# Performance work log

Hardware: AMD Instinct MI355X
Metric: run time of the kernel (lower is better)

Reference implementation:

```python
import jax, jax.numpy as jnp
import numpy as np

N = 32              # num_nodes
E = N * (N - 1)     # 992 directed edges
K = 2               # edge_types
D = 4               # n_in_node
H = 64              # msg_hid
M = 64              # msg_out
NH = 128            # n_hid
B, T = 8, 256


def setup_inputs() -> dict:
    key = jax.random.key(0)
    ks = jax.random.split(key, 14)
    # one-hot gather/scatter matrices over all ordered node pairs (i != j)
    pairs = np.array([(i, j) for i in range(N) for j in range(N) if i != j])
    eye = np.eye(N, dtype=np.float32)
    rel_rec = jnp.asarray(eye[pairs[:, 0]])   # [E, N] receiver one-hot
    rel_send = jnp.asarray(eye[pairs[:, 1]])  # [E, N] sender one-hot
    inputs = jax.random.normal(ks[0], (B, N, T, D), dtype=jnp.float32)
    s = 0.1
    return {
        "inputs": inputs,
        "rel_rec": rel_rec,
        "rel_send": rel_send,
        "rel_graph": jax.random.normal(ks[1], (1, 1, E, K), jnp.float32) * s,
        "W1": jax.random.normal(ks[2], (K, 2 * D, H), jnp.float32) * s,
        "b1": jnp.zeros((K, H), jnp.float32),
        "W2": jax.random.normal(ks[3], (K, H, M), jnp.float32) * s,
        "b2": jnp.zeros((K, M), jnp.float32),
        "Wo1": jax.random.normal(ks[4], (D + M, NH), jnp.float32) * s,
        "bo1": jnp.zeros((NH,), jnp.float32),
        "Wo2": jax.random.normal(ks[5], (NH, NH), jnp.float32) * s,
        "bo2": jnp.zeros((NH,), jnp.float32),
        "Wo3": jax.random.normal(ks[6], (NH, D), jnp.float32) * s,
        "bo3": jnp.zeros((D,), jnp.float32),
        "tau": 1,
        "hard": 1,
        "pred_steps": 1,
    }


def _single_step(x, rel_rec, rel_send, rel_graph, W1, b1, W2, b2,
                 Wo1, bo1, Wo2, bo2, Wo3, bo3):
    # x: [B, Tsub, N, D]
    receivers = jnp.einsum("en,btnd->bted", rel_rec, x)
    senders = jnp.einsum("en,btnd->bted", rel_send, x)
    pre_msg = jnp.concatenate([senders, receivers], axis=-1)  # [B,Tsub,E,2D]
    all_msgs = jnp.zeros(pre_msg.shape[:3] + (M,), pre_msg.dtype)
    for k in range(K):  # small fixed edge-type loop (dropout is identity, p=0)
        msg = jax.nn.relu(pre_msg @ W1[k] + b1[k])
        msg = jax.nn.relu(msg @ W2[k] + b2[k])          # [B,Tsub,E,M]
        all_msgs = all_msgs + msg * rel_graph[:, :, :, k:k + 1]
    # scatter back to receiver nodes: [B,Tsub,N,M]
    agg_msgs = jnp.einsum("btem,en->btnm", all_msgs, rel_rec)
    aug = jnp.concatenate([x, agg_msgs], axis=-1)
    pred = jax.nn.relu(aug @ Wo1 + bo1)
    pred = jax.nn.relu(pred @ Wo2 + bo2)
    pred = pred @ Wo3 + bo3
    return x + pred


def reference(inputs, rel_rec, rel_send, rel_graph, W1, b1, W2, b2,
              Wo1, bo1, Wo2, bo2, Wo3, bo3, tau, hard, pred_steps):
    # NOTE: original computes gumbel_softmax(rel_graph, tau, hard) but never
    # uses the result in the math, so tau/hard are inert here.
    x = jnp.transpose(inputs, (0, 2, 1, 3))  # [B, T, N, D]
    time_steps = x.shape[1]
    last_pred = x[:, ::pred_steps]           # [B, L, N, D]
    preds = []
    for _ in range(pred_steps):
        last_pred = _single_step(last_pred, rel_rec, rel_send, rel_graph,
                                 W1, b1, W2, b2, Wo1, bo1, Wo2, bo2, Wo3, bo3)
        preds.append(last_pred)
    Bx, L, Nn, Dd = preds[0].shape
    # interleave: output[:, i::pred_steps] = preds[i]
    output = jnp.stack(preds, axis=2).reshape(Bx, L * pred_steps, Nn, Dd)
    pred_all = output[:, : time_steps - 1]
    pred_all = jnp.transpose(pred_all, (0, 2, 1, 3))  # [B, N, T-1, D]
    rel_graph_out = jnp.broadcast_to(rel_graph[:, 0], (inputs.shape[0], E, K))
    return (pred_all, rel_graph_out)
```

## Files before the change

### kernel.cpp

```cpp
#include <hip/hip_runtime.h>


typedef _Float16     f16x8 __attribute__((ext_vector_type(8)));
typedef float        f32x4 __attribute__((ext_vector_type(4)));
typedef unsigned int u32x4 __attribute__((ext_vector_type(4)));

static __device__ __forceinline__ f16x8 pack8(float a0, float b0, float a1, float b1,
                                              float a2, float b2, float a3, float b3)
{
    u32x4 u;
    u.x = __builtin_bit_cast(unsigned int, __builtin_amdgcn_cvt_pkrtz(a0, b0));
    u.y = __builtin_bit_cast(unsigned int, __builtin_amdgcn_cvt_pkrtz(a1, b1));
    u.z = __builtin_bit_cast(unsigned int, __builtin_amdgcn_cvt_pkrtz(a2, b2));
    u.w = __builtin_bit_cast(unsigned int, __builtin_amdgcn_cvt_pkrtz(a3, b3));
    return __builtin_bit_cast(f16x8, u);
}

__global__ __launch_bounds__(256, 3)
void nri_fused(const float* __restrict__ inputs,
               const float* __restrict__ rgraph,
               const float* __restrict__ W1,  const float* __restrict__ b1,
               const float* __restrict__ W2,  const float* __restrict__ b2,
               const float* __restrict__ Wo1, const float* __restrict__ bo1,
               const float* __restrict__ Wo2, const float* __restrict__ bo2,
               const float* __restrict__ Wo3, const float* __restrict__ bo3,
               float* __restrict__ out)
{
    __shared__ float smem[11968];
    float* x_l = smem;
    float* g_l = smem + 128;
    float* S   = smem + 2112;
    float* R   = smem + 4288;
    float* aug = smem + 6464;
    _Float16* w2t = reinterpret_cast<_Float16*>(smem + 9664);
    _Float16* h_l = reinterpret_cast<_Float16*>(smem + 9664);
    float* p2  = smem + 2112;

    const int tid  = threadIdx.x;
    const int b    = blockIdx.x >> 8;
    const int t    = blockIdx.x & 255;
    const int w    = tid >> 6;
    const int lane = tid & 63;
    const int q    = lane & 15;
    const int g4   = lane >> 4;

    if (tid < 32)
        reinterpret_cast<float4*>(x_l)[tid] =
            *reinterpret_cast<const float4*>(inputs + ((size_t)(b * 32 + tid) * 256 + t) * 4);
    for (int idx = tid; idx < 1984; idx += 256) g_l[idx] = rgraph[idx];
    for (int idx = tid; idx < 1024; idx += 256) {
        const int n = idx >> 5, c = idx & 31;
        aug[n * 100 + 64 + c] =
            (c < 4) ? inputs[((size_t)(b * 32 + n) * 256 + t) * 4 + c] : 0.f;
    }

    float agg_acc[8];
    #pragma unroll
    for (int rr = 0; rr < 8; ++rr) agg_acc[rr] = 0.f;

    for (int k = 0; k < 2; ++k) {
        __syncthreads();
        for (int idx = tid; idx < 2048; idx += 256) {
            const int j = idx >> 6, kk = idx & 63;
            const float4 xj = reinterpret_cast<const float4*>(x_l)[j];
            const float* wp = W1 + k * 512 + kk;
            float s = b1[k * 64 + kk], r = 0.f;
            s = fmaf(xj.x, wp[0],   s);  r = fmaf(xj.x, wp[256], r);
            s = fmaf(xj.y, wp[64],  s);  r = fmaf(xj.y, wp[320], r);
            s = fmaf(xj.z, wp[128], s);  r = fmaf(xj.z, wp[384], r);
            s = fmaf(xj.w, wp[192], s);  r = fmaf(xj.w, wp[448], r);
            S[j * 68 + kk] = s;
            R[j * 68 + kk] = r;
        }
        for (int idx = tid; idx < 4096; idx += 256) {
            const int kk = idx >> 6, m = idx & 63;
            w2t[m * 72 + kk] = (_Float16)W2[k * 4096 + idx];
        }
        float bb[4];
        #pragma unroll
        for (int n = 0; n < 4; ++n) bb[n] = b2[k * 64 + 16 * n + q];
        __syncthreads();

        #pragma unroll
        for (int rr = 0; rr < 8; ++rr) {
            const int i = w * 8 + rr;
            f32x4 acc[2][4];
            #pragma unroll
            for (int m = 0; m < 2; ++m)
                #pragma unroll
                for (int n = 0; n < 4; ++n) {
                    acc[m][n][0] = bb[n]; acc[m][n][1] = bb[n];
                    acc[m][n][2] = bb[n]; acc[m][n][3] = bb[n];
                }
            #pragma unroll
            for (int s = 0; s < 2; ++s) {
                const float* rp = R + i * 68 + 32 * s + 8 * g4;
                const float4 Rv0 = *reinterpret_cast<const float4*>(rp);
                const float4 Rv1 = *reinterpret_cast<const float4*>(rp + 4);
                f16x8 af[2];
                #pragma unroll
                for (int m = 0; m < 2; ++m) {
                    const int r = 16 * m + q;
                    const int j = (r == 31) ? 0 : ((r < i) ? r : r + 1);
                    const float* sp = S + j * 68 + 32 * s + 8 * g4;
                    const float4 s0 = *reinterpret_cast<const float4*>(sp);
                    const float4 s1 = *reinterpret_cast<const float4*>(sp + 4);
                    af[m] = pack8(
                        fmaxf(s0.x + Rv0.x, 0.f), fmaxf(s0.y + Rv0.y, 0.f),
                        fmaxf(s0.z + Rv0.z, 0.f), fmaxf(s0.w + Rv0.w, 0.f),
                        fmaxf(s1.x + Rv1.x, 0.f), fmaxf(s1.y + Rv1.y, 0.f),
                        fmaxf(s1.z + Rv1.z, 0.f), fmaxf(s1.w + Rv1.w, 0.f));
                }
                #pragma unroll
                for (int n = 0; n < 4; ++n) {
                    const f16x8 wb = *reinterpret_cast<const f16x8*>(
                        w2t + (16 * n + q) * 72 + 32 * s + 8 * g4);
                    acc[0][n] = __builtin_amdgcn_mfma_f32_16x16x32_f16(
                        af[0], wb, acc[0][n], 0, 0, 0);
                    acc[1][n] = __builtin_amdgcn_mfma_f32_16x16x32_f16(
                        af[1], wb, acc[1][n], 0, 0, 0);
                }
            }
            float part[4] = {0.f, 0.f, 0.f, 0.f};
            #pragma unroll
            for (int m = 0; m < 2; ++m)
                #pragma unroll
                for (int reg = 0; reg < 4; ++reg) {
                    const int row = 16 * m + 4 * g4 + reg;
                    const float gv = (row < 31) ? g_l[(31 * i + row) * 2 + k] : 0.f;
                    #pragma unroll
                    for (int n = 0; n < 4; ++n)
                        part[n] = fmaf(fmaxf(acc[m][n][reg], 0.f), gv, part[n]);
                }
            #pragma unroll
            for (int n = 0; n < 4; ++n) {
                part[n] += __shfl_xor(part[n], 16);
                part[n] += __shfl_xor(part[n], 32);
            }
            const float v = (g4 == 0) ? part[0] : (g4 == 1) ? part[1]
                          : (g4 == 2) ? part[2] : part[3];
            agg_acc[rr] += v;
        }
    }

    #pragma unroll
    for (int rr = 0; rr < 8; ++rr)
        aug[(w * 8 + rr) * 100 + 16 * g4 + q] = agg_acc[rr];
    __syncthreads();

    const int c0 = 32 * w;

    {
        f16x8 bf[2][3];
        #pragma unroll
        for (int n = 0; n < 2; ++n)
            #pragma unroll
            for (int s = 0; s < 3; ++s) {
                const int col = c0 + 16 * n + q;
                const int ka = 32 * s + 8 * g4;
                float vv[8];
                #pragma unroll
                for (int e2 = 0; e2 < 8; ++e2) {
                    const int kx = ka + e2;
                    vv[e2] = (kx < 64) ? Wo1[(4 + kx) * 128 + col]
                           : ((kx < 68) ? Wo1[(kx - 64) * 128 + col] : 0.f);
                }
                bf[n][s] = pack8(vv[0], vv[1], vv[2], vv[3], vv[4], vv[5], vv[6], vv[7]);
            }
        f32x4 acc[2][2];
        #pragma unroll
        for (int m = 0; m < 2; ++m)
            #pragma unroll
            for (int n = 0; n < 2; ++n) {
                const float bv = bo1[c0 + 16 * n + q];
                acc[m][n][0] = bv; acc[m][n][1] = bv; acc[m][n][2] = bv; acc[m][n][3] = bv;
            }
        #pragma unroll
        for (int s = 0; s < 3; ++s) {
            f16x8 afr[2];
            #pragma unroll
            for (int m = 0; m < 2; ++m) {
                const float* ap = aug + (16 * m + q) * 100 + 32 * s + 8 * g4;
                const float4 a0 = *reinterpret_cast<const float4*>(ap);
                const float4 a1 = *reinterpret_cast<const float4*>(ap + 4);
                afr[m] = pack8(a0.x, a0.y, a0.z, a0.w, a1.x, a1.y, a1.z, a1.w);
            }
            #pragma unroll
            for (int m = 0; m < 2; ++m)
                #pragma unroll
                for (int n = 0; n < 2; ++n)
                    acc[m][n] = __builtin_amdgcn_mfma_f32_16x16x32_f16(
                        afr[m], bf[n][s], acc[m][n], 0, 0, 0);
        }
        __syncthreads();
        #pragma unroll
        for (int m = 0; m < 2; ++m)
            #pragma unroll
            for (int n = 0; n < 2; ++n)
                #pragma unroll
                for (int reg = 0; reg < 4; ++reg) {
                    const int row = 16 * m + 4 * g4 + reg;
                    h_l[row * 136 + c0 + 16 * n + q] = (_Float16)fmaxf(acc[m][n][reg], 0.f);
                }
    }
    __syncthreads();

    {
        f16x8 bf[2][4];
        #pragma unroll
        for (int n = 0; n < 2; ++n)
            #pragma unroll
            for (int s = 0; s < 4; ++s) {
                const int col = c0 + 16 * n + q;
                const int ka = 32 * s + 8 * g4;
                bf[n][s] = pack8(Wo2[(ka + 0) * 128 + col], Wo2[(ka + 1) * 128 + col],
                                 Wo2[(ka + 2) * 128 + col], Wo2[(ka + 3) * 128 + col],
                                 Wo2[(ka + 4) * 128 + col], Wo2[(ka + 5) * 128 + col],
                                 Wo2[(ka + 6) * 128 + col], Wo2[(ka + 7) * 128 + col]);
            }
        f32x4 acc[2][2];
        #pragma unroll
        for (int m = 0; m < 2; ++m)
            #pragma unroll
            for (int n = 0; n < 2; ++n) {
                const float bv = bo2[c0 + 16 * n + q];
                acc[m][n][0] = bv; acc[m][n][1] = bv; acc[m][n][2] = bv; acc[m][n][3] = bv;
            }
        #pragma unroll
        for (int s = 0; s < 4; ++s) {
            f16x8 afr[2];
            #pragma unroll
            for (int m = 0; m < 2; ++m)
                afr[m] = *reinterpret_cast<const f16x8*>(
                    h_l + (16 * m + q) * 136 + 32 * s + 8 * g4);
            #pragma unroll
            for (int m = 0; m < 2; ++m)
                #pragma unroll
                for (int n = 0; n < 2; ++n)
                    acc[m][n] = __builtin_amdgcn_mfma_f32_16x16x32_f16(
                        afr[m], bf[n][s], acc[m][n], 0, 0, 0);
        }
        #pragma unroll
        for (int m = 0; m < 2; ++m)
            #pragma unroll
            for (int n = 0; n < 2; ++n)
                #pragma unroll
                for (int reg = 0; reg < 4; ++reg) {
                    const int row = 16 * m + 4 * g4 + reg;
                    p2[row * 132 + c0 + 16 * n + q] = fmaxf(acc[m][n][reg], 0.f);
                }
    }
    __syncthreads();

    if (tid < 128 && t < 255) {
        const int rr3 = tid >> 2;
        const int dd  = tid & 3;
        float a0 = 0.f, a1 = 0.f, a2 = 0.f, a3 = 0.f;
        const float* pr = p2 + rr3 * 132;
        for (int d = 0; d < 128; d += 4) {
            a0 = fmaf(pr[d + 0], Wo3[(d + 0) * 4 + dd], a0);
            a1 = fmaf(pr[d + 1], Wo3[(d + 1) * 4 + dd], a1);
            a2 = fmaf(pr[d + 2], Wo3[(d + 2) * 4 + dd], a2);
            a3 = fmaf(pr[d + 3], Wo3[(d + 3) * 4 + dd], a3);
        }
        const float pred = ((a0 + a1) + (a2 + a3)) + bo3[dd];
        out[((size_t)(b * 32 + rr3) * 255 + t) * 4 + dd] = x_l[rr3 * 4 + dd] + pred;
    }
}

__global__ void copy_relgraph(const float* __restrict__ g, float* __restrict__ out2)
{
    const int idx = blockIdx.x * 256 + threadIdx.x;
    if (idx < 15872) out2[idx] = g[idx % 1984];
}

extern "C" void kernel_launch(void* const* d_in, const int* in_sizes, int n_in,
                              void* d_out, int out_size, void* d_ws, size_t ws_size,
                              hipStream_t stream)
{
    (void)in_sizes; (void)n_in; (void)d_ws; (void)ws_size; (void)out_size;
    const float* inputs    = (const float*)d_in[0];
    const float* rel_graph = (const float*)d_in[3];
    const float* W1  = (const float*)d_in[4];
    const float* b1  = (const float*)d_in[5];
    const float* W2  = (const float*)d_in[6];
    const float* b2  = (const float*)d_in[7];
    const float* Wo1 = (const float*)d_in[8];
    const float* bo1 = (const float*)d_in[9];
    const float* Wo2 = (const float*)d_in[10];
    const float* bo2 = (const float*)d_in[11];
    const float* Wo3 = (const float*)d_in[12];
    const float* bo3 = (const float*)d_in[13];
    float* out = (float*)d_out;

    nri_fused<<<2048, 256, 0, stream>>>(inputs, rel_graph, W1, b1, W2, b2,
                                        Wo1, bo1, Wo2, bo2, Wo3, bo3, out);
    copy_relgraph<<<62, 256, 0, stream>>>(rel_graph, out + 261120);
}
```

Measured before the change: 183.6 us.

## Shrink LDS and split MFMA accumulators to raise occupancy to four blocks

Raises launch bounds from 3 to 4 blocks per CU and shrinks shared memory. The rel_graph weights are now stored as fp16, and the aug buffer no longer holds the raw input columns; the last K-slice of the first output MLP instead reads x directly from x_l. The message MLP's second layer is split into two halves of output columns, so only 4 accumulators are live at once instead of 8, which cuts register pressure. A __syncthreads is removed. Risks include fp16 rounding of the graph weights and possible spills or a race from the removed barrier, since h_l aliases w2t.

Result: slower. 223.4 us (+21.7%).

```diff
diff --git a/kernel.cpp b/kernel.cpp
--- a/kernel.cpp
+++ b/kernel.cpp
@@ -16,7 +16,7 @@
     return __builtin_bit_cast(f16x8, u);
 }
 
-__global__ __launch_bounds__(256, 3)
+__global__ __launch_bounds__(256, 4)
 void nri_fused(const float* __restrict__ inputs,
                const float* __restrict__ rgraph,
                const float* __restrict__ W1,  const float* __restrict__ b1,
@@ -26,15 +26,15 @@
                const float* __restrict__ Wo3, const float* __restrict__ bo3,
                float* __restrict__ out)
 {
-    __shared__ float smem[11968];
+    __shared__ float smem[9952];
     float* x_l = smem;
-    float* g_l = smem + 128;
-    float* S   = smem + 2112;
-    float* R   = smem + 4288;
-    float* aug = smem + 6464;
-    _Float16* w2t = reinterpret_cast<_Float16*>(smem + 9664);
-    _Float16* h_l = reinterpret_cast<_Float16*>(smem + 9664);
-    float* p2  = smem + 2112;
+    _Float16* g16 = reinterpret_cast<_Float16*>(smem + 128);
+    float* S   = smem + 1120;
+    float* R   = smem + 3296;
+    float* aug = smem + 5472;
+    _Float16* w2t = reinterpret_cast<_Float16*>(smem + 7648);
+    _Float16* h_l = reinterpret_cast<_Float16*>(smem + 7648);
+    float* p2  = smem + 1120;
 
     const int tid  = threadIdx.x;
     const int b    = blockIdx.x >> 8;
@@ -47,12 +47,7 @@
     if (tid < 32)
         reinterpret_cast<float4*>(x_l)[tid] =
             *reinterpret_cast<const float4*>(inputs + ((size_t)(b * 32 + tid) * 256 + t) * 4);
-    for (int idx = tid; idx < 1984; idx += 256) g_l[idx] = rgraph[idx];
-    for (int idx = tid; idx < 1024; idx += 256) {
-        const int n = idx >> 5, c = idx & 31;
-        aug[n * 100 + 64 + c] =
-            (c < 4) ? inputs[((size_t)(b * 32 + n) * 256 + t) * 4 + c] : 0.f;
-    }
+    for (int idx = tid; idx < 1984; idx += 256) g16[idx] = (_Float16)rgraph[idx];
 
     float agg_acc[8];
     #pragma unroll
@@ -84,20 +79,12 @@
         #pragma unroll
         for (int rr = 0; rr < 8; ++rr) {
             const int i = w * 8 + rr;
-            f32x4 acc[2][4];
-            #pragma unroll
-            for (int m = 0; m < 2; ++m)
-                #pragma unroll
-                for (int n = 0; n < 4; ++n) {
-                    acc[m][n][0] = bb[n]; acc[m][n][1] = bb[n];
-                    acc[m][n][2] = bb[n]; acc[m][n][3] = bb[n];
-                }
+            f16x8 af[2][2];
             #pragma unroll
             for (int s = 0; s < 2; ++s) {
                 const float* rp = R + i * 68 + 32 * s + 8 * g4;
                 const float4 Rv0 = *reinterpret_cast<const float4*>(rp);
                 const float4 Rv1 = *reinterpret_cast<const float4*>(rp + 4);
-                f16x8 af[2];
                 #pragma unroll
                 for (int m = 0; m < 2; ++m) {
                     const int r = 16 * m + q;
@@ -105,33 +92,57 @@
                     const float* sp = S + j * 68 + 32 * s + 8 * g4;
                     const float4 s0 = *reinterpret_cast<const float4*>(sp);
                     const float4 s1 = *reinterpret_cast<const float4*>(sp + 4);
-                    af[m] = pack8(
+                    af[m][s] = pack8(
                         fmaxf(s0.x + Rv0.x, 0.f), fmaxf(s0.y + Rv0.y, 0.f),
                         fmaxf(s0.z + Rv0.z, 0.f), fmaxf(s0.w + Rv0.w, 0.f),
                         fmaxf(s1.x + Rv1.x, 0.f), fmaxf(s1.y + Rv1.y, 0.f),
                         fmaxf(s1.z + Rv1.z, 0.f), fmaxf(s1.w + Rv1.w, 0.f));
                 }
-                #pragma unroll
-                for (int n = 0; n < 4; ++n) {
-                    const f16x8 wb = *reinterpret_cast<const f16x8*>(
-                        w2t + (16 * n + q) * 72 + 32 * s + 8 * g4);
-                    acc[0][n] = __builtin_amdgcn_mfma_f32_16x16x32_f16(
-                        af[0], wb, acc[0][n], 0, 0, 0);
-                    acc[1][n] = __builtin_amdgcn_mfma_f32_16x16x32_f16(
-                        af[1], wb, acc[1][n], 0, 0, 0);
-                }
-            }
-            float part[4] = {0.f, 0.f, 0.f, 0.f};
+            }
+            float gvr[8];
             #pragma unroll
             for (int m = 0; m < 2; ++m)
                 #pragma unroll
                 for (int reg = 0; reg < 4; ++reg) {
                     const int row = 16 * m + 4 * g4 + reg;
-                    const float gv = (row < 31) ? g_l[(31 * i + row) * 2 + k] : 0.f;
+                    gvr[m * 4 + reg] =
+                        (row < 31) ? (float)g16[(31 * i + row) * 2 + k] : 0.f;
+                }
+            float part[4];
+            #pragma unroll
+            for (int nh = 0; nh < 2; ++nh) {
+                f32x4 acc[2][2];
+                #pragma unroll
+                for (int m = 0; m < 2; ++m)
                     #pragma unroll
-                    for (int n = 0; n < 4; ++n)
-                        part[n] = fmaf(fmaxf(acc[m][n][reg], 0.f), gv, part[n]);
-                }
+                    for (int n2 = 0; n2 < 2; ++n2) {
+                        const float bv = bb[2 * nh + n2];
+                        acc[m][n2][0] = bv; acc[m][n2][1] = bv;
+                        acc[m][n2][2] = bv; acc[m][n2][3] = bv;
+                    }
+                #pragma unroll
+                for (int s = 0; s < 2; ++s)
+                    #pragma unroll
+                    for (int n2 = 0; n2 < 2; ++n2) {
+                        const f16x8 wb = *reinterpret_cast<const f16x8*>(
+                            w2t + (16 * (2 * nh + n2) + q) * 72 + 32 * s + 8 * g4);
+                        acc[0][n2] = __builtin_amdgcn_mfma_f32_16x16x32_f16(
+                            af[0][s], wb, acc[0][n2], 0, 0, 0);
+                        acc[1][n2] = __builtin_amdgcn_mfma_f32_16x16x32_f16(
+                            af[1][s], wb, acc[1][n2], 0, 0, 0);
+                    }
+                float p0 = 0.f, p1 = 0.f;
+                #pragma unroll
+                for (int m = 0; m < 2; ++m)
+                    #pragma unroll
+                    for (int reg = 0; reg < 4; ++reg) {
+                        const float gv = gvr[m * 4 + reg];
+                        p0 = fmaf(fmaxf(acc[m][0][reg], 0.f), gv, p0);
+                        p1 = fmaf(fmaxf(acc[m][1][reg], 0.f), gv, p1);
+                    }
+                part[2 * nh + 0] = p0;
+                part[2 * nh + 1] = p1;
+            }
             #pragma unroll
             for (int n = 0; n < 4; ++n) {
                 part[n] += __shfl_xor(part[n], 16);
@@ -145,7 +156,7 @@
 
     #pragma unroll
     for (int rr = 0; rr < 8; ++rr)
-        aug[(w * 8 + rr) * 100 + 16 * g4 + q] = agg_acc[rr];
+        aug[(w * 8 + rr) * 68 + 16 * g4 + q] = agg_acc[rr];
     __syncthreads();
 
     const int c0 = 32 * w;
@@ -176,11 +187,11 @@
                 acc[m][n][0] = bv; acc[m][n][1] = bv; acc[m][n][2] = bv; acc[m][n][3] = bv;
             }
         #pragma unroll
-        for (int s = 0; s < 3; ++s) {
+        for (int s = 0; s < 2; ++s) {
             f16x8 afr[2];
             #pragma unroll
             for (int m = 0; m < 2; ++m) {
-                const float* ap = aug + (16 * m + q) * 100 + 32 * s + 8 * g4;
+                const float* ap = aug + (16 * m + q) * 68 + 32 * s + 8 * g4;
                 const float4 a0 = *reinterpret_cast<const float4*>(ap);
                 const float4 a1 = *reinterpret_cast<const float4*>(ap + 4);
                 afr[m] = pack8(a0.x, a0.y, a0.z, a0.w, a1.x, a1.y, a1.z, a1.w);
@@ -192,7 +203,23 @@
                     acc[m][n] = __builtin_amdgcn_mfma_f32_16x16x32_f16(
                         afr[m], bf[n][s], acc[m][n], 0, 0, 0);
         }
-        __syncthreads();
+        {
+            const f16x8 zero8 = __builtin_bit_cast(f16x8, (u32x4){0u, 0u, 0u, 0u});
+            f16x8 afr[2];
+            #pragma unroll
+            for (int m = 0; m < 2; ++m) {
+                const float4 xr = *reinterpret_cast<const float4*>(x_l + (16 * m + q) * 4);
+                afr[m] = (g4 == 0)
+                    ? pack8(xr.x, xr.y, xr.z, xr.w, 0.f, 0.f, 0.f, 0.f)
+                    : zero8;
+            }
+            #pragma unroll
+            for (int m = 0; m < 2; ++m)
+                #pragma unroll
+                for (int n = 0; n < 2; ++n)
+                    acc[m][n] = __builtin_amdgcn_mfma_f32_16x16x32_f16(
+                        afr[m], bf[n][2], acc[m][n], 0, 0, 0);
+        }
         #pragma unroll
         for (int m = 0; m < 2; ++m)
             #pragma unroll
```
